# Performance work log

Measured on AMD Instinct MI355X. Metric: run time of the kernel, lower is better.

Reference implementation:

```python
import jax, jax.numpy as jnp
import numpy as np

DIM = 512
DIM_TIME = 64
DIM_FF = 2048
B, L = 2, 512
EPS = 1e-5


def _layer_norm(x, g, b):
    mu = jnp.mean(x, axis=-1, keepdims=True)
    var = jnp.mean((x - mu) ** 2, axis=-1, keepdims=True)
    return (x - mu) * jax.lax.rsqrt(var + EPS) * g + b


def _sioconv(u, wa, hid_re, hid_im):
    # u: (B, L, Dt) float. Faithful to the FFT/triu construction, expressed as
    # cumulative log-sums (linear conv with all-ones == causal cumsum).
    Bb, Ll, Dt = u.shape
    out = (u @ wa.T).reshape(Bb, Ll, Dt, 2)          # linear_a, view_as_complex
    a_sqr = out[..., 0] ** 2 + out[..., 1] ** 2
    a = (out[..., 0] + 1j * out[..., 1]) * (jax.lax.rsqrt(a_sqr) * jnp.exp(-a_sqr))
    a = jnp.transpose(a, (0, 2, 1))                  # (B, Dt, L)
    a_ln = jnp.log(a)
    S = jnp.cumsum(a_ln, axis=-1)                    # S_k = sum_{j<=k} ln a_j
    S_prev = jnp.concatenate([jnp.zeros_like(S[..., :1]), S[..., :-1]], axis=-1)
    # c[b,d,i,k] = exp(S_k - S_{i-1}) = prod_{j=i..k} a_j, kept for k >= i-1
    diff = S[:, :, None, :] - S_prev[:, :, :, None]  # (B, Dt, L, L)
    idx = jnp.arange(Ll)
    mask = idx[None, :] >= (idx[:, None] - 1)        # k >= i-1 (triu diag=-1)
    c = jnp.where(mask, jnp.exp(diff), 0.0)
    uc = jnp.transpose(u.astype(jnp.complex64), (0, 2, 1))   # (B, Dt, L)
    hidden = (hid_re + 1j * hid_im)[None, :] * jnp.ones((Bb, 1), jnp.complex64)
    xin = jnp.concatenate([hidden[..., None], uc[..., :-1]], axis=-1)  # rolled + h0
    h = jnp.einsum('bdik,bdk->bdi', c, xin)
    h = h.at[:, :, -1].add(uc[:, :, -1])
    return jnp.transpose(h.real, (0, 2, 1)).astype(u.dtype)


def _ffn(x, w1, b1, w2, b2):
    return jax.nn.silu(x @ w1.T + b1) @ w2.T + b2


def setup_inputs() -> dict:
    key = jax.random.key(0)
    ks = jax.random.split(key, 12)
    d, dt, dff = DIM, DIM_TIME, DIM_FF
    return {
        'x': jax.random.normal(ks[0], (B, L, d), jnp.float32),
        'ln1_g': jnp.ones((d,), jnp.float32), 'ln1_b': jnp.zeros((d,), jnp.float32),
        'fc_w': jax.random.normal(ks[1], (dt, d), jnp.float32) * d ** -0.5,
        'fc_b': jnp.zeros((dt,), jnp.float32),
        'lin_in_w': jax.random.normal(ks[2], (dt, d), jnp.float32) * d ** -0.5,
        'lin_in_b': jnp.zeros((dt,), jnp.float32),
        'wa': jax.random.normal(ks[3], (2 * dt, dt), jnp.float32) * dt ** -0.5,
        'hid_re': jax.random.normal(ks[4], (dt,), jnp.float32),
        'hid_im': jax.random.normal(ks[5], (dt,), jnp.float32),
        'lin_out_w': jax.random.normal(ks[6], (d, dt), jnp.float32) * dt ** -0.5,
        'lin_out_b': jnp.zeros((d,), jnp.float32),
        'ln2_g': jnp.ones((d,), jnp.float32), 'ln2_b': jnp.zeros((d,), jnp.float32),
        'w1': jax.random.normal(ks[7], (dff, d), jnp.float32) * d ** -0.5,
        'b1': jnp.zeros((dff,), jnp.float32),
        'w2': jax.random.normal(ks[8], (d, dff), jnp.float32) * dff ** -0.5,
        'b2': jnp.zeros((d,), jnp.float32),
    }


def reference(x, ln1_g, ln1_b, fc_w, fc_b, lin_in_w, lin_in_b, wa, hid_re, hid_im,
              lin_out_w, lin_out_b, ln2_g, ln2_b, w1, b1, w2, b2):
    x_res = x
    xn = _layer_norm(x, ln1_g, ln1_b)
    y = jax.nn.silu(xn @ fc_w.T + fc_b)                  # gate, (B, L, Dt)
    u = xn @ lin_in_w.T + lin_in_b                       # (B, L, Dt)
    h = _sioconv(u, wa, hid_re, hid_im)
    x = (h * y) @ lin_out_w.T + lin_out_b + x_res        # dropout = identity (eval)
    x_res = x
    x = _ffn(_layer_norm(x, ln2_g, ln2_b), w1, b1, w2, b2) + x_res
    return x
```

## Files before the change

### kernel.cpp

```cpp
#include <hip/hip_runtime.h>
#include <math.h>

#define LSEQ 512
#define DMODEL 512
#define DT 64
#define DFF 2048

typedef unsigned short u16;
typedef __attribute__((ext_vector_type(8))) short short8;
typedef __attribute__((ext_vector_type(4))) float f32x4;

__device__ __forceinline__ float wave_sum(float v) {
#pragma unroll
  for (int o = 32; o > 0; o >>= 1) v += __shfl_xor(v, o, 64);
  return v;
}

__device__ __forceinline__ u16 f2bf(float f) {
  unsigned int u = __float_as_uint(f);
  u += 0x7fffu + ((u >> 16) & 1u);
  return (u16)(u >> 16);
}
__device__ __forceinline__ float bf2f(u16 h) {
  return __uint_as_float(((unsigned int)h) << 16);
}
__device__ __forceinline__ void splitbf(float f, u16& h, u16& l) {
  h = f2bf(f);
  l = f2bf(f - bf2f(h));
}

__device__ __forceinline__ void gload_lds16(const void* g, void* l) {
  __builtin_amdgcn_global_load_lds(
      (const __attribute__((address_space(1))) unsigned int*)g,
      (__attribute__((address_space(3))) unsigned int*)l, 16, 0, 0);
}

__global__ __launch_bounds__(256) void k_cvtall(
    const float* __restrict__ w1, const float* __restrict__ w2,
    const float* __restrict__ fcw, const float* __restrict__ liw,
    const float* __restrict__ wa, const float* __restrict__ low,
    u16* __restrict__ w1b, u16* __restrict__ w2b,
    u16* __restrict__ fclh, u16* __restrict__ fcll,
    u16* __restrict__ wah, u16* __restrict__ wal,
    u16* __restrict__ lowh, u16* __restrict__ lowl)
{
  int i = blockIdx.x * 256 + threadIdx.x;
  if (i >= 550912) return;
  if (i < 524288) {
    const float* s = (i < 262144) ? w1 : w2;
    u16* d = (i < 262144) ? w1b : w2b;
    int off = (i < 262144) ? i : i - 262144;
    float4 v = ((const float4*)s)[off];
    ushort4 o;
    o.x = f2bf(v.x); o.y = f2bf(v.y); o.z = f2bf(v.z); o.w = f2bf(v.w);
    ((ushort4*)d)[off] = o;
    return;
  }
  const float* s; int j; u16 *dh, *dl;
  if (i < 532480)      { s = fcw; j = i - 524288;        dh = fclh; dl = fcll; }
  else if (i < 540672) { s = liw; j = i - 532480 + 8192; dh = fclh; dl = fcll; }
  else if (i < 542720) { s = wa;  j = i - 540672;        dh = wah;  dl = wal;  }
  else                 { s = low; j = i - 542720;        dh = lowh; dl = lowl; }
  int soff = (i < 532480) ? i - 524288 :
             (i < 540672) ? i - 532480 :
             (i < 542720) ? i - 540672 : i - 542720;
  float4 v = ((const float4*)s)[soff];
  ushort4 oh, ol;
  splitbf(v.x, oh.x, ol.x); splitbf(v.y, oh.y, ol.y);
  splitbf(v.z, oh.z, ol.z); splitbf(v.w, oh.w, ol.w);
  ((ushort4*)dh)[j] = oh;
  ((ushort4*)dl)[j] = ol;
}

template<int LO>
__global__ __launch_bounds__(256) void k_ln(
    const float* __restrict__ in, const float* __restrict__ g,
    const float* __restrict__ be, u16* __restrict__ outh, u16* __restrict__ outl)
{
  const int lane = threadIdx.x & 63, wv = threadIdx.x >> 6;
  const int row = blockIdx.x * 4 + wv;
  const float* xr = in + (size_t)row * DMODEL;
  float v[8]; float s = 0.f;
#pragma unroll
  for (int j = 0; j < 8; ++j) { v[j] = xr[lane + 64 * j]; s += v[j]; }
  s = wave_sum(s);
  const float mu = s * (1.f / 512.f);
  float q = 0.f;
#pragma unroll
  for (int j = 0; j < 8; ++j) { float dd = v[j] - mu; q += dd * dd; }
  q = wave_sum(q);
  const float rstd = rsqrtf(q * (1.f / 512.f) + 1e-5f);
#pragma unroll
  for (int j = 0; j < 8; ++j) {
    int idx = lane + 64 * j;
    float o = (v[j] - mu) * rstd * g[idx] + be[idx];
    if constexpr (LO) {
      u16 h, l; splitbf(o, h, l);
      outh[(size_t)row * DMODEL + idx] = h;
      outl[(size_t)row * DMODEL + idx] = l;
    } else {
      outh[(size_t)row * DMODEL + idx] = f2bf(o);
    }
  }
}

__global__ __launch_bounds__(256) void k_proj(
    const u16* __restrict__ xnh, const u16* __restrict__ xnl,
    const u16* __restrict__ fclh, const u16* __restrict__ fcll,
    const float* __restrict__ fcb, const float* __restrict__ lib,
    float* __restrict__ y_o, float* __restrict__ u_o,
    u16* __restrict__ ubh, u16* __restrict__ ubl)
{
  const int w = threadIdx.x >> 6, lane = threadIdx.x & 63;
  const int mt = blockIdx.x, nt = blockIdx.y * 4 + w;
  const int lr = lane & 15, lk = lane >> 4;
  const size_t aoff = (size_t)(mt * 16 + lr) * DMODEL + lk * 8;
  const size_t boff = (size_t)(nt * 16 + lr) * DMODEL + lk * 8;
  f32x4 acc = {};
#pragma unroll 4
  for (int k = 0; k < DMODEL; k += 32) {
    short8 ah = *(const short8*)(xnh + aoff + k);
    short8 al = *(const short8*)(xnl + aoff + k);
    short8 bh = *(const short8*)(fclh + boff + k);
    short8 bl = *(const short8*)(fcll + boff + k);
    acc = __builtin_amdgcn_mfma_f32_16x16x32_bf16(ah, bh, acc, 0, 0, 0);
    acc = __builtin_amdgcn_mfma_f32_16x16x32_bf16(ah, bl, acc, 0, 0, 0);
    acc = __builtin_amdgcn_mfma_f32_16x16x32_bf16(al, bh, acc, 0, 0, 0);
  }
  const int c = nt * 16 + lr;
#pragma unroll
  for (int j = 0; j < 4; ++j) {
    int row = mt * 16 + lk * 4 + j;
    float v = acc[j];
    if (c < DT) {
      v += fcb[c];
      y_o[row * DT + c] = v / (1.f + expf(-v));
    } else {
      int d = c - DT;
      v += lib[d];
      u_o[row * DT + d] = v;
      u16 h, l; splitbf(v, h, l);
      ubh[row * DT + d] = h;
      ubl[row * DT + d] = l;
    }
  }
}

__global__ __launch_bounds__(256) void k_au(
    const u16* __restrict__ ubh, const u16* __restrict__ ubl,
    const u16* __restrict__ wah, const u16* __restrict__ wal,
    float* __restrict__ ar_o, float* __restrict__ ai_o)
{
  const int w = threadIdx.x >> 6, lane = threadIdx.x & 63;
  const int mt = blockIdx.x, nt = blockIdx.y * 4 + w;
  const int lr = lane & 15, lk = lane >> 4;
  const size_t aoff = (size_t)(mt * 16 + lr) * DT + lk * 8;
  const size_t boff = (size_t)(nt * 16 + lr) * DT + lk * 8;
  f32x4 acc = {};
#pragma unroll
  for (int k = 0; k < DT; k += 32) {
    short8 ah = *(const short8*)(ubh + aoff + k);
    short8 al = *(const short8*)(ubl + aoff + k);
    short8 bh = *(const short8*)(wah + boff + k);
    short8 bl = *(const short8*)(wal + boff + k);
    acc = __builtin_amdgcn_mfma_f32_16x16x32_bf16(ah, bh, acc, 0, 0, 0);
    acc = __builtin_amdgcn_mfma_f32_16x16x32_bf16(ah, bl, acc, 0, 0, 0);
    acc = __builtin_amdgcn_mfma_f32_16x16x32_bf16(al, bh, acc, 0, 0, 0);
  }
  const int c = nt * 16 + lr;
#pragma unroll
  for (int j = 0; j < 4; ++j) {
    float v = acc[j];
    float p = __shfl_xor(v, 1, 64);
    float re = (lane & 1) ? p : v;
    float im = (lane & 1) ? v : p;
    float asq = re * re + im * im;
    float sc = rsqrtf(asq) * expf(-asq);
    int row = mt * 16 + lk * 4 + j;
    int d = c >> 1;
    if (lane & 1) ai_o[row * DT + d] = im * sc;
    else          ar_o[row * DT + d] = re * sc;
  }
}

__global__ __launch_bounds__(64) void k_scan2(
    const float* __restrict__ u, const float* __restrict__ ar, const float* __restrict__ ai,
    const float* __restrict__ hr, const float* __restrict__ hi, float* __restrict__ h_o)
{
  const int blk = blockIdx.x;
  const int b = blk >> 6, d = blk & 63;
  const int lane = threadIdx.x;
  const size_t base = (size_t)b * LSEQ * DT + d;
  const int i0 = lane * 8;

  float a_r[8], a_i[8], b_r[8], b_i[8];
#pragma unroll
  for (int e = 0; e < 8; ++e) {
    int i = i0 + e;
    a_r[e] = ar[base + (size_t)i * DT];
    a_i[e] = ai[base + (size_t)i * DT];
    if (i >= 2)      { b_r[e] = u[base + (size_t)(i - 2) * DT]; b_i[e] = 0.f; }
    else if (i == 1) { b_r[e] = hr[d]; b_i[e] = hi[d]; }
    else             { b_r[e] = 0.f;   b_i[e] = 0.f; }
  }

  float Ar = 1.f, Ai = 0.f, Br = 0.f, Bi = 0.f;
#pragma unroll
  for (int e = 0; e < 8; ++e) {
    float nBr = fmaf(Ar, b_r[e], fmaf(-Ai, b_i[e], Br));
    float nBi = fmaf(Ar, b_i[e], fmaf( Ai, b_r[e], Bi));
    float nAr = Ar * a_r[e] - Ai * a_i[e];
    float nAi = Ar * a_i[e] + Ai * a_r[e];
    Ar = nAr; Ai = nAi; Br = nBr; Bi = nBi;
  }

#pragma unroll
  for (int dlt = 1; dlt < 64; dlt <<= 1) {
    float Ar2 = __shfl_down(Ar, dlt, 64);
    float Ai2 = __shfl_down(Ai, dlt, 64);
    float Br2 = __shfl_down(Br, dlt, 64);
    float Bi2 = __shfl_down(Bi, dlt, 64);
    if (lane + dlt < 64) {
      float nAr = Ar * Ar2 - Ai * Ai2;
      float nAi = Ar * Ai2 + Ai * Ar2;
      float nBr = fmaf(Ar, Br2, fmaf(-Ai, Bi2, Br));
      float nBi = fmaf(Ar, Bi2, fmaf( Ai, Br2, Bi));
      Ar = nAr; Ai = nAi; Br = nBr; Bi = nBi;
    }
  }

  float A1r = __shfl_down(Ar, 1, 64), A1i = __shfl_down(Ai, 1, 64);
  float B1r = __shfl_down(Br, 1, 64), B1i = __shfl_down(Bi, 1, 64);
  if (lane == 63) { A1r = 1.f; A1i = 0.f; B1r = 0.f; B1i = 0.f; }
  const float r512 = u[base + (size_t)(LSEQ - 2) * DT];
  float rr = fmaf(A1r, r512, B1r);
  float ri = fmaf(A1i, r512, B1i);

  const float uL = u[base + (size_t)(LSEQ - 1) * DT];
#pragma unroll
  for (int e = 7; e >= 0; --e) {
    int i = i0 + e;
    float nr = fmaf(a_r[e], rr, fmaf(-a_i[e], ri, b_r[e]));
    float ni = fmaf(a_r[e], ri, fmaf( a_i[e], rr, b_i[e]));
    rr = nr; ri = ni;
    float outv = rr;
    if (i == LSEQ - 1) outv += uL;
    h_o[base + (size_t)i * DT] = outv;
  }
}

__global__ __launch_bounds__(256) void k_mid2(
    const float* __restrict__ h, const float* __restrict__ y,
    const u16* __restrict__ lowh, const u16* __restrict__ lowl,
    const float* __restrict__ lob, const float* __restrict__ x,
    float* __restrict__ x2_o)
{
  const int w = threadIdx.x >> 6, lane = threadIdx.x & 63;
  const int mt = blockIdx.x, nt = blockIdx.y * 4 + w;
  const int lr = lane & 15, lk = lane >> 4;
  const int arow = mt * 16 + lr;
  const float* hp = h + (size_t)arow * DT + lk * 8;
  const float* yp = y + (size_t)arow * DT + lk * 8;
  const size_t boff = (size_t)(nt * 16 + lr) * DT + lk * 8;
  f32x4 acc = {};
#pragma unroll
  for (int ks = 0; ks < 2; ++ks) {
    float4 h0 = *(const float4*)(hp + ks * 32);
    float4 h1 = *(const float4*)(hp + ks * 32 + 4);
    float4 y0 = *(const float4*)(yp + ks * 32);
    float4 y1 = *(const float4*)(yp + ks * 32 + 4);
    float pv[8] = {h0.x * y0.x, h0.y * y0.y, h0.z * y0.z, h0.w * y0.w,
                   h1.x * y1.x, h1.y * y1.y, h1.z * y1.z, h1.w * y1.w};
    short8 ah, al;
#pragma unroll
    for (int e = 0; e < 8; ++e) {
      u16 hh, ll; splitbf(pv[e], hh, ll);
      ah[e] = (short)hh; al[e] = (short)ll;
    }
    short8 bh = *(const short8*)(lowh + boff + ks * 32);
    short8 bl = *(const short8*)(lowl + boff + ks * 32);
    acc = __builtin_amdgcn_mfma_f32_16x16x32_bf16(ah, bh, acc, 0, 0, 0);
    acc = __builtin_amdgcn_mfma_f32_16x16x32_bf16(ah, bl, acc, 0, 0, 0);
    acc = __builtin_amdgcn_mfma_f32_16x16x32_bf16(al, bh, acc, 0, 0, 0);
  }
  const int c = nt * 16 + lr;
#pragma unroll
  for (int j = 0; j < 4; ++j) {
    int row = mt * 16 + lk * 4 + j;
    x2_o[(size_t)row * DMODEL + c] = acc[j] + lob[c] + x[(size_t)row * DMODEL + c];
  }
}

template<int BM, int BN, int EPI>
__global__ __launch_bounds__(256) void k_mfma(
    const u16* __restrict__ A, const u16* __restrict__ B,
    const float* __restrict__ bias, float* __restrict__ Cf, u16* __restrict__ Cb,
    int K, int N, int kTiles, int partStride)
{
  constexpr int MF = BM / 32, NF = BN / 32;
  __shared__ __align__(16) u16 As[BM * 64];
  __shared__ __align__(16) u16 Bs[BN * 64];
  const int t = threadIdx.x;
  const int m0 = blockIdx.x * BM, n0 = blockIdx.y * BN;
  const int kBase = blockIdx.z * kTiles * 64;
  const int w = t >> 6, lane = t & 63;
  const int wm = w >> 1, wn = w & 1;
  const int lr = lane & 15, lk = lane >> 4;
  f32x4 acc[MF][NF] = {};

  for (int kt = 0; kt < kTiles; ++kt) {
    const int k0 = kBase + kt * 64;
#pragma unroll
    for (int i = 0; i < BM / 32; ++i) {
      int e = i * 2048 + t * 8;
      int row = e >> 6, col = e & 63;
      gload_lds16(A + (size_t)(m0 + row) * K + k0 + col, &As[e]);
    }
#pragma unroll
    for (int i = 0; i < BN / 32; ++i) {
      int e = i * 2048 + t * 8;
      int row = e >> 6, col = e & 63;
      gload_lds16(B + (size_t)(n0 + row) * K + k0 + col, &Bs[e]);
    }
    __syncthreads();
#pragma unroll
    for (int ks = 0; ks < 2; ++ks) {
      short8 af[MF], bf[NF];
#pragma unroll
      for (int mf = 0; mf < MF; ++mf)
        af[mf] = *(const short8*)&As[(wm * (BM / 2) + mf * 16 + lr) * 64 + ks * 32 + lk * 8];
#pragma unroll
      for (int nf = 0; nf < NF; ++nf)
        bf[nf] = *(const short8*)&Bs[(wn * (BN / 2) + nf * 16 + lr) * 64 + ks * 32 + lk * 8];
#pragma unroll
      for (int mf = 0; mf < MF; ++mf)
#pragma unroll
        for (int nf = 0; nf < NF; ++nf)
          acc[mf][nf] = __builtin_amdgcn_mfma_f32_16x16x32_bf16(af[mf], bf[nf], acc[mf][nf], 0, 0, 0);
    }
    __syncthreads();
  }

#pragma unroll
  for (int mf = 0; mf < MF; ++mf)
#pragma unroll
    for (int nf = 0; nf < NF; ++nf)
#pragma unroll
      for (int j = 0; j < 4; ++j) {
        int rrow = m0 + wm * (BM / 2) + mf * 16 + lk * 4 + j;
        int ccol = n0 + wn * (BN / 2) + nf * 16 + lr;
        if constexpr (EPI == 0) {
          float v = acc[mf][nf][j] + bias[ccol];
          v = v / (1.f + expf(-v));
          Cb[(size_t)rrow * N + ccol] = f2bf(v);
        } else {
          Cf[(size_t)blockIdx.z * partStride + (size_t)rrow * N + ccol] = acc[mf][nf][j];
        }
      }
}

__global__ __launch_bounds__(256) void k_red(
    const float* __restrict__ p, const float* __restrict__ b2,
    const float* __restrict__ x2, float* __restrict__ out, int n4, int partStride4)
{
  int i = blockIdx.x * 256 + threadIdx.x;
  if (i >= n4) return;
  const float4* p4 = (const float4*)p;
  float4 s = p4[i];
  float4 s1 = p4[i + partStride4];
  float4 s2 = p4[i + 2 * partStride4];
  float4 s3 = p4[i + 3 * partStride4];
  s.x += s1.x; s.y += s1.y; s.z += s1.z; s.w += s1.w;
  s.x += s2.x; s.y += s2.y; s.z += s2.z; s.w += s2.w;
  s.x += s3.x; s.y += s3.y; s.z += s3.z; s.w += s3.w;
  int col4 = i & 127;
  float4 bb = ((const float4*)b2)[col4];
  float4 rr = ((const float4*)x2)[i];
  s.x += bb.x + rr.x; s.y += bb.y + rr.y; s.z += bb.z + rr.z; s.w += bb.w + rr.w;
  ((float4*)out)[i] = s;
}

extern "C" void kernel_launch(void* const* d_in, const int* in_sizes, int n_in,
                              void* d_out, int out_size, void* d_ws, size_t ws_size,
                              hipStream_t stream) {
  const float* x    = (const float*)d_in[0];
  const float* ln1g = (const float*)d_in[1];
  const float* ln1b = (const float*)d_in[2];
  const float* fcw  = (const float*)d_in[3];
  const float* fcb  = (const float*)d_in[4];
  const float* liw  = (const float*)d_in[5];
  const float* lib  = (const float*)d_in[6];
  const float* wa   = (const float*)d_in[7];
  const float* hidr = (const float*)d_in[8];
  const float* hidi = (const float*)d_in[9];
  const float* low  = (const float*)d_in[10];
  const float* lob  = (const float*)d_in[11];
  const float* ln2g = (const float*)d_in[12];
  const float* ln2b = (const float*)d_in[13];
  const float* w1   = (const float*)d_in[14];
  const float* b1   = (const float*)d_in[15];
  const float* w2   = (const float*)d_in[16];
  const float* b2   = (const float*)d_in[17];
  float* out = (float*)d_out;
  float* ws  = (float*)d_ws;

  const int R = 2 * LSEQ;
  float* y_    = ws;
  float* u_    = y_   + 65536;
  float* ar_   = u_   + 65536;
  float* ai_   = ar_  + 65536;
  float* h_    = ai_  + 65536;
  float* x2_   = h_   + 65536;
  float* part_ = x2_  + 524288;
  u16* p = (u16*)(part_ + 2097152);
  u16* xnh  = p;            p += 524288;
  u16* xnl  = p;            p += 524288;
  u16* xn2b = p;            p += 524288;
  u16* ubh  = p;            p += 65536;
  u16* ubl  = p;            p += 65536;
  u16* h1b  = p;            p += 2097152;
  u16* w1b  = p;            p += 1048576;
  u16* w2b  = p;            p += 1048576;
  u16* fclh = p;            p += 65536;
  u16* fcll = p;            p += 65536;
  u16* wah  = p;            p += 8192;
  u16* wal  = p;            p += 8192;
  u16* lowh = p;            p += 32768;
  u16* lowl = p;            p += 32768;

  k_cvtall<<<2152, 256, 0, stream>>>(w1, w2, fcw, liw, wa, low,
                                     w1b, w2b, fclh, fcll, wah, wal, lowh, lowl);
  k_ln<1><<<256, 256, 0, stream>>>(x, ln1g, ln1b, xnh, xnl);
  k_proj<<<dim3(64, 2), 256, 0, stream>>>(xnh, xnl, fclh, fcll, fcb, lib,
                                          y_, u_, ubh, ubl);
  k_au<<<dim3(64, 2), 256, 0, stream>>>(ubh, ubl, wah, wal, ar_, ai_);
  k_scan2<<<128, 64, 0, stream>>>(u_, ar_, ai_, hidr, hidi, h_);
  k_mid2<<<dim3(64, 8), 256, 0, stream>>>(h_, y_, lowh, lowl, lob, x, x2_);
  k_ln<0><<<256, 256, 0, stream>>>(x2_, ln2g, ln2b, xn2b, nullptr);
  dim3 g1(R / 64, DFF / 64);
  k_mfma<64, 64, 0><<<g1, 256, 0, stream>>>(xn2b, w1b, b1, nullptr, h1b,
                                            DMODEL, DFF, DMODEL / 64, 0);
  dim3 g2(R / 64, DMODEL / 64, 4);
  k_mfma<64, 64, 2><<<g2, 256, 0, stream>>>(h1b, w2b, nullptr, part_, nullptr,
                                            DFF, DMODEL, (DFF / 4) / 64, R * DMODEL);
  k_red<<<(R * DMODEL / 4 + 255) / 256, 256, 0, stream>>>(part_, b2, x2_, out,
                                                          R * DMODEL / 4, R * DMODEL / 4);
}
```

Before: 62.47 us.

## Fuse LN1 into weight conversion, proj with a-gen, and out-proj with LN2

Cuts the launch count from nine kernels to six. LayerNorm1 runs as extra blocks inside the weight-conversion kernel. The gate/input projection and the complex-a projection are fused into one kernel that hands u through LDS instead of global bf16 buffers. The output projection, residual add and LayerNorm2 are fused per 16-row tile in a 1024-thread block that keeps x2 in LDS. The aim is to save launch overhead and global round-trips, at the cost of fewer, larger blocks (64 blocks), which lowers parallelism in the fused stages.

New measurement: 64.74 us. 1.04x slower.

```diff
diff --git a/kernel.cpp b/kernel.cpp
--- a/kernel.cpp
+++ b/kernel.cpp
@@ -35,15 +35,42 @@
       (__attribute__((address_space(3))) unsigned int*)l, 16, 0, 0);
 }
 
-__global__ __launch_bounds__(256) void k_cvtall(
+__global__ __launch_bounds__(256) void k_pre(
     const float* __restrict__ w1, const float* __restrict__ w2,
     const float* __restrict__ fcw, const float* __restrict__ liw,
     const float* __restrict__ wa, const float* __restrict__ low,
+    const float* __restrict__ x, const float* __restrict__ g1,
+    const float* __restrict__ be1,
     u16* __restrict__ w1b, u16* __restrict__ w2b,
     u16* __restrict__ fclh, u16* __restrict__ fcll,
     u16* __restrict__ wah, u16* __restrict__ wal,
-    u16* __restrict__ lowh, u16* __restrict__ lowl)
-{
+    u16* __restrict__ lowh, u16* __restrict__ lowl,
+    u16* __restrict__ xnh, u16* __restrict__ xnl)
+{
+  if (blockIdx.x >= 2152) {
+    const int lane = threadIdx.x & 63, wv = threadIdx.x >> 6;
+    const int row = (blockIdx.x - 2152) * 4 + wv;
+    const float* xr = x + (size_t)row * DMODEL;
+    float v[8]; float s = 0.f;
+#pragma unroll
+    for (int j = 0; j < 8; ++j) { v[j] = xr[lane + 64 * j]; s += v[j]; }
+    s = wave_sum(s);
+    const float mu = s * (1.f / 512.f);
+    float q = 0.f;
+#pragma unroll
+    for (int j = 0; j < 8; ++j) { float dd = v[j] - mu; q += dd * dd; }
+    q = wave_sum(q);
+    const float rstd = rsqrtf(q * (1.f / 512.f) + 1e-5f);
+#pragma unroll
+    for (int j = 0; j < 8; ++j) {
+      int idx = lane + 64 * j;
+      float o = (v[j] - mu) * rstd * g1[idx] + be1[idx];
+      u16 h, l; splitbf(o, h, l);
+      xnh[(size_t)row * DMODEL + idx] = h;
+      xnl[(size_t)row * DMODEL + idx] = l;
+    }
+    return;
+  }
   int i = blockIdx.x * 256 + threadIdx.x;
   if (i >= 550912) return;
   if (i < 524288) {
@@ -72,114 +99,80 @@
   ((ushort4*)dl)[j] = ol;
 }
 
-template<int LO>
-__global__ __launch_bounds__(256) void k_ln(
-    const float* __restrict__ in, const float* __restrict__ g,
-    const float* __restrict__ be, u16* __restrict__ outh, u16* __restrict__ outl)
-{
-  const int lane = threadIdx.x & 63, wv = threadIdx.x >> 6;
-  const int row = blockIdx.x * 4 + wv;
-  const float* xr = in + (size_t)row * DMODEL;
-  float v[8]; float s = 0.f;
-#pragma unroll
-  for (int j = 0; j < 8; ++j) { v[j] = xr[lane + 64 * j]; s += v[j]; }
-  s = wave_sum(s);
-  const float mu = s * (1.f / 512.f);
-  float q = 0.f;
-#pragma unroll
-  for (int j = 0; j < 8; ++j) { float dd = v[j] - mu; q += dd * dd; }
-  q = wave_sum(q);
-  const float rstd = rsqrtf(q * (1.f / 512.f) + 1e-5f);
-#pragma unroll
-  for (int j = 0; j < 8; ++j) {
-    int idx = lane + 64 * j;
-    float o = (v[j] - mu) * rstd * g[idx] + be[idx];
-    if constexpr (LO) {
-      u16 h, l; splitbf(o, h, l);
-      outh[(size_t)row * DMODEL + idx] = h;
-      outl[(size_t)row * DMODEL + idx] = l;
-    } else {
-      outh[(size_t)row * DMODEL + idx] = f2bf(o);
-    }
-  }
-}
-
-__global__ __launch_bounds__(256) void k_proj(
+__global__ __launch_bounds__(512) void k_fa(
     const u16* __restrict__ xnh, const u16* __restrict__ xnl,
     const u16* __restrict__ fclh, const u16* __restrict__ fcll,
+    const u16* __restrict__ wah, const u16* __restrict__ wal,
     const float* __restrict__ fcb, const float* __restrict__ lib,
     float* __restrict__ y_o, float* __restrict__ u_o,
-    u16* __restrict__ ubh, u16* __restrict__ ubl)
-{
+    float* __restrict__ ar_o, float* __restrict__ ai_o)
+{
+  __shared__ __align__(16) u16 ush[16][80];
+  __shared__ __align__(16) u16 usl[16][80];
   const int w = threadIdx.x >> 6, lane = threadIdx.x & 63;
-  const int mt = blockIdx.x, nt = blockIdx.y * 4 + w;
+  const int mt = blockIdx.x;
   const int lr = lane & 15, lk = lane >> 4;
-  const size_t aoff = (size_t)(mt * 16 + lr) * DMODEL + lk * 8;
-  const size_t boff = (size_t)(nt * 16 + lr) * DMODEL + lk * 8;
-  f32x4 acc = {};
+
+  {
+    const size_t aoff = (size_t)(mt * 16 + lr) * DMODEL + lk * 8;
+    const size_t boff = (size_t)(w * 16 + lr) * DMODEL + lk * 8;
+    f32x4 acc = {};
 #pragma unroll 4
-  for (int k = 0; k < DMODEL; k += 32) {
-    short8 ah = *(const short8*)(xnh + aoff + k);
-    short8 al = *(const short8*)(xnl + aoff + k);
-    short8 bh = *(const short8*)(fclh + boff + k);
-    short8 bl = *(const short8*)(fcll + boff + k);
-    acc = __builtin_amdgcn_mfma_f32_16x16x32_bf16(ah, bh, acc, 0, 0, 0);
-    acc = __builtin_amdgcn_mfma_f32_16x16x32_bf16(ah, bl, acc, 0, 0, 0);
-    acc = __builtin_amdgcn_mfma_f32_16x16x32_bf16(al, bh, acc, 0, 0, 0);
-  }
-  const int c = nt * 16 + lr;
-#pragma unroll
-  for (int j = 0; j < 4; ++j) {
-    int row = mt * 16 + lk * 4 + j;
-    float v = acc[j];
-    if (c < DT) {
-      v += fcb[c];
-      y_o[row * DT + c] = v / (1.f + expf(-v));
-    } else {
-      int d = c - DT;
-      v += lib[d];
-      u_o[row * DT + d] = v;
-      u16 h, l; splitbf(v, h, l);
-      ubh[row * DT + d] = h;
-      ubl[row * DT + d] = l;
-    }
-  }
-}
-
-__global__ __launch_bounds__(256) void k_au(
-    const u16* __restrict__ ubh, const u16* __restrict__ ubl,
-    const u16* __restrict__ wah, const u16* __restrict__ wal,
-    float* __restrict__ ar_o, float* __restrict__ ai_o)
-{
-  const int w = threadIdx.x >> 6, lane = threadIdx.x & 63;
-  const int mt = blockIdx.x, nt = blockIdx.y * 4 + w;
-  const int lr = lane & 15, lk = lane >> 4;
-  const size_t aoff = (size_t)(mt * 16 + lr) * DT + lk * 8;
-  const size_t boff = (size_t)(nt * 16 + lr) * DT + lk * 8;
-  f32x4 acc = {};
-#pragma unroll
-  for (int k = 0; k < DT; k += 32) {
-    short8 ah = *(const short8*)(ubh + aoff + k);
-    short8 al = *(const short8*)(ubl + aoff + k);
-    short8 bh = *(const short8*)(wah + boff + k);
-    short8 bl = *(const short8*)(wal + boff + k);
-    acc = __builtin_amdgcn_mfma_f32_16x16x32_bf16(ah, bh, acc, 0, 0, 0);
-    acc = __builtin_amdgcn_mfma_f32_16x16x32_bf16(ah, bl, acc, 0, 0, 0);
-    acc = __builtin_amdgcn_mfma_f32_16x16x32_bf16(al, bh, acc, 0, 0, 0);
-  }
-  const int c = nt * 16 + lr;
-#pragma unroll
-  for (int j = 0; j < 4; ++j) {
-    float v = acc[j];
-    float p = __shfl_xor(v, 1, 64);
-    float re = (lane & 1) ? p : v;
-    float im = (lane & 1) ? v : p;
-    float asq = re * re + im * im;
-    float sc = rsqrtf(asq) * expf(-asq);
-    int row = mt * 16 + lk * 4 + j;
-    int d = c >> 1;
-    if (lane & 1) ai_o[row * DT + d] = im * sc;
-    else          ar_o[row * DT + d] = re * sc;
+    for (int k = 0; k < DMODEL; k += 32) {
+      short8 ah = *(const short8*)(xnh + aoff + k);
+      short8 al = *(const short8*)(xnl + aoff + k);
+      short8 bh = *(const short8*)(fclh + boff + k);
+      short8 bl = *(const short8*)(fcll + boff + k);
+      acc = __builtin_amdgcn_mfma_f32_16x16x32_bf16(ah, bh, acc, 0, 0, 0);
+      acc = __builtin_amdgcn_mfma_f32_16x16x32_bf16(ah, bl, acc, 0, 0, 0);
+      acc = __builtin_amdgcn_mfma_f32_16x16x32_bf16(al, bh, acc, 0, 0, 0);
+    }
+    const int c = w * 16 + lr;
+#pragma unroll
+    for (int j = 0; j < 4; ++j) {
+      int rl = lk * 4 + j;
+      int row = mt * 16 + rl;
+      float v = acc[j];
+      if (c < DT) {
+        v += fcb[c];
+        y_o[row * DT + c] = v / (1.f + expf(-v));
+      } else {
+        int d = c - DT;
+        v += lib[d];
+        u_o[row * DT + d] = v;
+        u16 h, l; splitbf(v, h, l);
+        ush[rl][d] = h; usl[rl][d] = l;
+      }
+    }
+  }
+  __syncthreads();
+  {
+    const size_t boff = (size_t)(w * 16 + lr) * DT + lk * 8;
+    f32x4 acc = {};
+#pragma unroll
+    for (int ks = 0; ks < 2; ++ks) {
+      short8 ah = *(const short8*)&ush[lr][ks * 32 + lk * 8];
+      short8 al = *(const short8*)&usl[lr][ks * 32 + lk * 8];
+      short8 bh = *(const short8*)(wah + boff + ks * 32);
+      short8 bl = *(const short8*)(wal + boff + ks * 32);
+      acc = __builtin_amdgcn_mfma_f32_16x16x32_bf16(ah, bh, acc, 0, 0, 0);
+      acc = __builtin_amdgcn_mfma_f32_16x16x32_bf16(ah, bl, acc, 0, 0, 0);
+      acc = __builtin_amdgcn_mfma_f32_16x16x32_bf16(al, bh, acc, 0, 0, 0);
+    }
+    const int c = w * 16 + lr;
+#pragma unroll
+    for (int j = 0; j < 4; ++j) {
+      float v = acc[j];
+      float p = __shfl_xor(v, 1, 64);
+      float re = (lane & 1) ? p : v;
+      float im = (lane & 1) ? v : p;
+      float asq = re * re + im * im;
+      float sc = rsqrtf(asq) * expf(-asq);
+      int row = mt * 16 + lk * 4 + j;
+      int d = c >> 1;
+      if (lane & 1) ai_o[row * DT + d] = im * sc;
+      else          ar_o[row * DT + d] = re * sc;
+    }
   }
 }
 
@@ -249,45 +242,75 @@
   }
 }
 
-__global__ __launch_bounds__(256) void k_mid2(
+__global__ __launch_bounds__(1024) void k_midln(
     const float* __restrict__ h, const float* __restrict__ y,
     const u16* __restrict__ lowh, const u16* __restrict__ lowl,
     const float* __restrict__ lob, const float* __restrict__ x,
-    float* __restrict__ x2_o)
-{
-  const int w = threadIdx.x >> 6, lane = threadIdx.x & 63;
-  const int mt = blockIdx.x, nt = blockIdx.y * 4 + w;
+    const float* __restrict__ g2, const float* __restrict__ be2,
+    float* __restrict__ x2_o, u16* __restrict__ xn2b)
+{
+  __shared__ __align__(16) u16 hyh[16][80];
+  __shared__ __align__(16) u16 hyl[16][80];
+  __shared__ float x2s[16][520];
+  const int tid = threadIdx.x;
+  const int w = tid >> 6, lane = tid & 63;
   const int lr = lane & 15, lk = lane >> 4;
-  const int arow = mt * 16 + lr;
-  const float* hp = h + (size_t)arow * DT + lk * 8;
-  const float* yp = y + (size_t)arow * DT + lk * 8;
-  const size_t boff = (size_t)(nt * 16 + lr) * DT + lk * 8;
-  f32x4 acc = {};
-#pragma unroll
-  for (int ks = 0; ks < 2; ++ks) {
-    float4 h0 = *(const float4*)(hp + ks * 32);
-    float4 h1 = *(const float4*)(hp + ks * 32 + 4);
-    float4 y0 = *(const float4*)(yp + ks * 32);
-    float4 y1 = *(const float4*)(yp + ks * 32 + 4);
-    float pv[8] = {h0.x * y0.x, h0.y * y0.y, h0.z * y0.z, h0.w * y0.w,
-                   h1.x * y1.x, h1.y * y1.y, h1.z * y1.z, h1.w * y1.w};
-    short8 ah, al;
-#pragma unroll
-    for (int e = 0; e < 8; ++e) {
-      u16 hh, ll; splitbf(pv[e], hh, ll);
-      ah[e] = (short)hh; al[e] = (short)ll;
-    }
-    short8 bh = *(const short8*)(lowh + boff + ks * 32);
-    short8 bl = *(const short8*)(lowl + boff + ks * 32);
-    acc = __builtin_amdgcn_mfma_f32_16x16x32_bf16(ah, bh, acc, 0, 0, 0);
-    acc = __builtin_amdgcn_mfma_f32_16x16x32_bf16(ah, bl, acc, 0, 0, 0);
-    acc = __builtin_amdgcn_mfma_f32_16x16x32_bf16(al, bh, acc, 0, 0, 0);
-  }
-  const int c = nt * 16 + lr;
-#pragma unroll
-  for (int j = 0; j < 4; ++j) {
-    int row = mt * 16 + lk * 4 + j;
-    x2_o[(size_t)row * DMODEL + c] = acc[j] + lob[c] + x[(size_t)row * DMODEL + c];
+  const int mt = blockIdx.x;
+
+  {
+    int r = tid >> 6, d = tid & 63;
+    int row = mt * 16 + r;
+    float v = h[row * DT + d] * y[row * DT + d];
+    u16 hh, ll; splitbf(v, hh, ll);
+    hyh[r][d] = hh; hyl[r][d] = ll;
+  }
+  __syncthreads();
+
+#pragma unroll
+  for (int t = 0; t < 2; ++t) {
+    const int nt = w * 2 + t;
+    const size_t boff = (size_t)(nt * 16 + lr) * DT + lk * 8;
+    f32x4 acc = {};
+#pragma unroll
+    for (int ks = 0; ks < 2; ++ks) {
+      short8 ah = *(const short8*)&hyh[lr][ks * 32 + lk * 8];
+      short8 al = *(const short8*)&hyl[lr][ks * 32 + lk * 8];
+      short8 bh = *(const short8*)(lowh + boff + ks * 32);
+      short8 bl = *(const short8*)(lowl + boff + ks * 32);
+      acc = __builtin_amdgcn_mfma_f32_16x16x32_bf16(ah, bh, acc, 0, 0, 0);
+      acc = __builtin_amdgcn_mfma_f32_16x16x32_bf16(ah, bl, acc, 0, 0, 0);
+      acc = __builtin_amdgcn_mfma_f32_16x16x32_bf16(al, bh, acc, 0, 0, 0);
+    }
+    const int c = nt * 16 + lr;
+#pragma unroll
+    for (int j = 0; j < 4; ++j) {
+      int rl = lk * 4 + j;
+      int row = mt * 16 + rl;
+      float v = acc[j] + lob[c] + x[(size_t)row * DMODEL + c];
+      x2s[rl][c] = v;
+      x2_o[(size_t)row * DMODEL + c] = v;
+    }
+  }
+  __syncthreads();
+
+  {
+    const int r = w;
+    const int row = mt * 16 + r;
+    float v[8]; float s = 0.f;
+#pragma unroll
+    for (int j = 0; j < 8; ++j) { v[j] = x2s[r][lane + 64 * j]; s += v[j]; }
+    s = wave_sum(s);
+    const float mu = s * (1.f / 512.f);
+    float q = 0.f;
+#pragma unroll
+    for (int j = 0; j < 8; ++j) { float dd = v[j] - mu; q += dd * dd; }
+    q = wave_sum(q);
+    const float rstd = rsqrtf(q * (1.f / 512.f) + 1e-5f);
+#pragma unroll
+    for (int j = 0; j < 8; ++j) {
+      int idx = lane + 64 * j;
+      xn2b[(size_t)row * DMODEL + idx] = f2bf((v[j] - mu) * rstd * g2[idx] + be2[idx]);
+    }
   }
 }
 
@@ -416,8 +439,6 @@
   u16* xnh  = p;            p += 524288;
   u16* xnl  = p;            p += 524288;
   u16* xn2b = p;            p += 524288;
-  u16* ubh  = p;            p += 65536;
-  u16* ubl  = p;            p += 65536;
   u16* h1b  = p;            p += 2097152;
   u16* w1b  = p;            p += 1048576;
   u16* w2b  = p;            p += 1048576;
@@ -428,15 +449,14 @@
   u16* lowh = p;            p += 32768;
   u16* lowl = p;            p += 32768;
 
-  k_cvtall<<<2152, 256, 0, stream>>>(w1, w2, fcw, liw, wa, low,
-                                     w1b, w2b, fclh, fcll, wah, wal, lowh, lowl);
-  k_ln<1><<<256, 256, 0, stream>>>(x, ln1g, ln1b, xnh, xnl);
-  k_proj<<<dim3(64, 2), 256, 0, stream>>>(xnh, xnl, fclh, fcll, fcb, lib,
-                                          y_, u_, ubh, ubl);
-  k_au<<<dim3(64, 2), 256, 0, stream>>>(ubh, ubl, wah, wal, ar_, ai_);
+  k_pre<<<2408, 256, 0, stream>>>(w1, w2, fcw, liw, wa, low, x, ln1g, ln1b,
+                                  w1b, w2b, fclh, fcll, wah, wal, lowh, lowl,
+                                  xnh, xnl);
+  k_fa<<<64, 512, 0, stream>>>(xnh, xnl, fclh, fcll, wah, wal, fcb, lib,
+                               y_, u_, ar_, ai_);
   k_scan2<<<128, 64, 0, stream>>>(u_, ar_, ai_, hidr, hidi, h_);
-  k_mid2<<<dim3(64, 8), 256, 0, stream>>>(h_, y_, lowh, lowl, lob, x, x2_);
-  k_ln<0><<<256, 256, 0, stream>>>(x2_, ln2g, ln2b, xn2b, nullptr);
+  k_midln<<<64, 1024, 0, stream>>>(h_, y_, lowh, lowl, lob, x, ln2g, ln2b,
+                                   x2_, xn2b);
   dim3 g1(R / 64, DFF / 64);
   k_mfma<64, 64, 0><<<g1, 256, 0, stream>>>(xn2b, w1b, b1, nullptr, h1b,
                                             DMODEL, DFF, DMODEL / 64, 0);
```
